# Optimization experiments

Measured on AMD Instinct MI355X. Metric: run time of the kernel, lower is better.

Reference implementation:

```python
import jax, jax.numpy as jnp
import numpy as np

ATT, WEMB, VIEW, ADIM, EMB = 312, 512, 16, 2048, 2048
B = 2048
IN = ATT + WEMB + VIEW * WEMB  # 9016; output_dim defaults to input_dim
EPS = 1e-8  # torch cosine_similarity eps


def setup_inputs() -> dict:
    key = jax.random.key(0)
    ks = jax.random.split(key, 8)
    s = 0.02
    return {
        "x": jax.random.normal(ks[0], (B, IN), dtype=jnp.float32),
        "Wq": s * jax.random.normal(ks[1], (WEMB, ADIM), dtype=jnp.float32),
        "bq": jnp.zeros((ADIM,), jnp.float32),
        "Wk": s * jax.random.normal(ks[2], (WEMB, ADIM), dtype=jnp.float32),
        "bk": jnp.zeros((ADIM,), jnp.float32),
        "Wv": s * jax.random.normal(ks[3], (WEMB, ADIM), dtype=jnp.float32),
        "bv": jnp.zeros((ADIM,), jnp.float32),
        "Wm": s * jax.random.normal(ks[4], (ATT + ADIM, EMB), dtype=jnp.float32),
        "bm": jnp.zeros((EMB,), jnp.float32),
        "Wd1": s * jax.random.normal(ks[5], (EMB, 4096), dtype=jnp.float32),
        "bd1": jnp.zeros((4096,), jnp.float32),
        "Wd2": s * jax.random.normal(ks[6], (4096, IN), dtype=jnp.float32),
        "bd2": jnp.zeros((IN,), jnp.float32),
    }


def reference(x, Wq, bq, Wk, bk, Wv, bv, Wm, bm, Wd1, bd1, Wd2, bd2):
    att_emb = x[:, :ATT]                                   # [B, 312]
    desc_emb = x[:, ATT:ATT + WEMB]                        # [B, 512]
    gpt_emb = x[:, ATT + WEMB:].reshape(x.shape[0], -1, WEMB)  # [B, V, 512]

    # q is the same projected desc for every view (expand before linear)
    q = desc_emb @ Wq + bq                                 # [B, A]
    k = jnp.einsum("bvw,wa->bva", gpt_emb, Wk) + bk        # [B, V, A]
    v = jnp.einsum("bvw,wa->bva", gpt_emb, Wv) + bv        # [B, V, A]

    # cosed score: cosine similarity * L2 distance
    dot = jnp.einsum("bva,ba->bv", k, q)                   # [B, V]
    qn = jnp.maximum(jnp.linalg.norm(q, axis=-1), EPS)     # [B]
    kn = jnp.maximum(jnp.linalg.norm(k, axis=-1), EPS)     # [B, V]
    cs = dot / (qn[:, None] * kn)
    ed = jnp.linalg.norm(q[:, None, :] - k, axis=-1)       # [B, V]
    attn = jax.nn.softmax(cs * ed, axis=-1)                # [B, V]

    # torch.matmul([B,V], [B,V,A]) -> [B,B,A]; .mean(dim=1) averages over the
    # attn-batch axis, i.e. fused[j] = mean_b(attn[b]) @ v[j]. Compute the
    # mathematically identical form without the BxBxA intermediate.
    attn_mean = attn.mean(axis=0)                          # [V]
    fused = jnp.einsum("v,bva->ba", attn_mean, v)          # [B, A]

    z = jax.nn.relu(jnp.concatenate([att_emb, fused], axis=1) @ Wm + bm)  # [B, EMB]
    h = jax.nn.relu(z @ Wd1 + bd1)                          # [B, 4096]
    return h @ Wd2 + bd2                                    # [B, IN]
```

## Files before the change

kernel.cpp:

```cpp
#include <hip/hip_runtime.h>


typedef __bf16 bf16x8 __attribute__((ext_vector_type(8)));
typedef float  f32x4  __attribute__((ext_vector_type(4)));
typedef unsigned short u16;

#define ATT   312
#define WEMB  512
#define VIEW  16
#define ADIM  2048
#define EMB   2048
#define BATCH 2048
#define INDIM 9016
#define KCAT  2360
#define KCATP 2432
#define NOUT  9016
#define NOUTP 9088

__device__ __forceinline__ u16 f2bf(float f) {
  unsigned u = __builtin_bit_cast(unsigned, f);
  u += 0x7FFFu + ((u >> 16) & 1u);
  return (u16)(u >> 16);
}

__device__ __forceinline__ void gl_lds16(const u16* g, u16* l) {
  __builtin_amdgcn_global_load_lds((const __attribute__((address_space(1))) void*)g,
                                   (__attribute__((address_space(3))) void*)l, 16, 0, 0);
}

__global__ void castx_k(const float* __restrict__ x, u16* __restrict__ cc,
                        u16* __restrict__ desc, u16* __restrict__ gpt) {
  const int b = blockIdx.x, t = threadIdx.x;
  const float4* row = (const float4*)(x + (size_t)b * INDIM);
  for (int c = t; c < INDIM / 4; c += 256) {
    float4 v = row[c];
    ushort4 o = make_ushort4(f2bf(v.x), f2bf(v.y), f2bf(v.z), f2bf(v.w));
    if (c < ATT / 4)                 *(ushort4*)&cc[(size_t)b * KCATP + c * 4] = o;
    else if (c < (ATT + WEMB) / 4)   *(ushort4*)&desc[(size_t)b * WEMB + (c - ATT / 4) * 4] = o;
    else                             *(ushort4*)&gpt[(size_t)b * (VIEW * WEMB) + (c - (ATT + WEMB) / 4) * 4] = o;
  }
}

__global__ void transcast_k(const float* __restrict__ src, u16* __restrict__ dst,
                            int K, int N, int Kp, int Np) {
  __shared__ float tile[64][65];
  const int k0 = blockIdx.y * 64, n0 = blockIdx.x * 64;
  const int t = threadIdx.x;
  const int tr = t >> 4, tc4 = (t & 15) * 4;
#pragma unroll
  for (int i = 0; i < 4; ++i) {
    const int k = k0 + tr + i * 16;
    float v0 = 0.f, v1 = 0.f, v2 = 0.f, v3 = 0.f;
    if (k < K) {
      const int n = n0 + tc4;
      const float* p = src + (size_t)k * N + n;
      if (n + 3 < N) { float4 v = *(const float4*)p; v0 = v.x; v1 = v.y; v2 = v.z; v3 = v.w; }
      else {
        if (n + 0 < N) v0 = p[0];
        if (n + 1 < N) v1 = p[1];
        if (n + 2 < N) v2 = p[2];
        if (n + 3 < N) v3 = p[3];
      }
    }
    tile[tr + i * 16][tc4 + 0] = v0;
    tile[tr + i * 16][tc4 + 1] = v1;
    tile[tr + i * 16][tc4 + 2] = v2;
    tile[tr + i * 16][tc4 + 3] = v3;
  }
  __syncthreads();
#pragma unroll
  for (int i = 0; i < 4; ++i) {
    const int rn = tr + i * 16;
    const int n = n0 + rn;
    const int kk = k0 + tc4;
    if (n < Np) {
      const bool nv = (n < N);
      ushort4 o = make_ushort4(f2bf(nv ? tile[tc4 + 0][rn] : 0.f),
                               f2bf(nv ? tile[tc4 + 1][rn] : 0.f),
                               f2bf(nv ? tile[tc4 + 2][rn] : 0.f),
                               f2bf(nv ? tile[tc4 + 3][rn] : 0.f));
      *(ushort4*)&dst[(size_t)n * Kp + kk] = o;
    }
  }
}

template <int MODE, bool RELU>
__global__ __launch_bounds__(256, 2)
void gemm_bt(const u16* __restrict__ A, const u16* __restrict__ BT,
             const float* __restrict__ bias, int K, int Nreal,
             float* __restrict__ dstF, u16* __restrict__ dstH, int ldc,
             const float* __restrict__ qbuf, float* __restrict__ dotb,
             float* __restrict__ kn2b, int mt, int nt, int fastm) {
  __shared__ alignas(16) u16 Ash[128 * 64];
  __shared__ alignas(16) u16 Bsh[128 * 64];
  const int nwg = mt * nt;
  const int xcd = blockIdx.x & 7, idx = blockIdx.x >> 3;
  const int qq = nwg >> 3, rr = nwg & 7;
  const int wg = (xcd < rr ? xcd * (qq + 1) : rr * (qq + 1) + (xcd - rr) * qq) + idx;
  int tm, tn;
  if (fastm) { tm = wg % mt; tn = wg / mt; } else { tn = wg % nt; tm = wg / nt; }

  const int tid = threadIdx.x;
  const int wave = tid >> 6, lane = tid & 63;
  const long m0 = (long)tm * 128;
  const long n0 = (long)tn * 128;
  const int wm = wave >> 1, wn = wave & 1;
  f32x4 acc[4][4] = {};

  const int srow = (wave << 5) + (lane >> 3);
  const int scol = (lane & 7) << 3;

  for (int k0 = 0; k0 < K; k0 += 64) {
    __syncthreads();
#pragma unroll
    for (int i = 0; i < 4; ++i) {
      const int r = srow + i * 8;
      gl_lds16(A + (m0 + r) * (long)K + k0 + scol, &Ash[r * 64 + scol]);
      gl_lds16(BT + (n0 + r) * (long)K + k0 + scol, &Bsh[r * 64 + scol]);
    }
    __syncthreads();
#pragma unroll
    for (int kb = 0; kb < 2; ++kb) {
      bf16x8 af[4], bfv[4];
#pragma unroll
      for (int f = 0; f < 4; ++f) {
        af[f]  = *(const bf16x8*)&Ash[(wm * 64 + f * 16 + (lane & 15)) * 64 + kb * 32 + (lane >> 4) * 8];
        bfv[f] = *(const bf16x8*)&Bsh[(wn * 64 + f * 16 + (lane & 15)) * 64 + kb * 32 + (lane >> 4) * 8];
      }
#pragma unroll
      for (int mf = 0; mf < 4; ++mf)
#pragma unroll
        for (int nf = 0; nf < 4; ++nf)
          acc[mf][nf] = __builtin_amdgcn_mfma_f32_16x16x32_bf16(af[mf], bfv[nf], acc[mf][nf], 0, 0, 0);
    }
  }

  const int lr = lane >> 4, lc = lane & 15;
  if (MODE == 2) {
#pragma unroll
    for (int mf = 0; mf < 4; ++mf) {
#pragma unroll
      for (int r = 0; r < 4; ++r) {
        const long grow = m0 + wm * 64 + mf * 16 + lr * 4 + r;
        const long b = grow >> 4;
        float ds = 0.f, ks = 0.f;
#pragma unroll
        for (int nf = 0; nf < 4; ++nf) {
          const long col = n0 + wn * 64 + nf * 16 + lc;
          float kv = acc[mf][nf][r] + bias[col];
          ds += kv * qbuf[b * ADIM + col];
          ks += kv * kv;
        }
#pragma unroll
        for (int m = 1; m < 16; m <<= 1) {
          ds += __shfl_xor(ds, m, 64);
          ks += __shfl_xor(ks, m, 64);
        }
        if (lc == 0) {
          atomicAdd(&dotb[grow], ds);
          atomicAdd(&kn2b[grow], ks);
        }
      }
    }
  } else {
#pragma unroll
    for (int mf = 0; mf < 4; ++mf) {
#pragma unroll
      for (int nf = 0; nf < 4; ++nf) {
        const long col = n0 + wn * 64 + nf * 16 + lc;
        if (col < Nreal) {
          const float bv_ = bias[col];
#pragma unroll
          for (int r = 0; r < 4; ++r) {
            const long row = m0 + wm * 64 + mf * 16 + lr * 4 + r;
            float v = acc[mf][nf][r] + bv_;
            if (RELU) v = fmaxf(v, 0.f);
            if (MODE == 0) dstF[row * (long)ldc + col] = v;
            else           dstH[row * (long)ldc + col] = f2bf(v);
          }
        }
      }
    }
  }
}

__global__ void qnorm_k(const float* __restrict__ q, float* __restrict__ qn2) {
  const int b = blockIdx.x, t = threadIdx.x;
  const float4* row = (const float4*)(q + (size_t)b * ADIM);
  float s = 0.f;
#pragma unroll
  for (int i = 0; i < 2; ++i) {
    float4 v = row[t + i * 256];
    s += v.x * v.x + v.y * v.y + v.z * v.z + v.w * v.w;
  }
#pragma unroll
  for (int m = 1; m < 64; m <<= 1) s += __shfl_xor(s, m, 64);
  __shared__ float wsum[4];
  if ((t & 63) == 0) wsum[t >> 6] = s;
  __syncthreads();
  if (t == 0) qn2[b] = wsum[0] + wsum[1] + wsum[2] + wsum[3];
}

__global__ void attn_k(const float* __restrict__ dotb, const float* __restrict__ kn2b,
                       const float* __restrict__ qn2, float* __restrict__ asum) {
  const int b = blockIdx.x * 256 + threadIdx.x;
  const int lane = threadIdx.x & 63;
  const float q2 = qn2[b];
  const float qn = fmaxf(sqrtf(q2), 1e-8f);
  float lg[VIEW];
  float mx = -1e30f;
#pragma unroll
  for (int v = 0; v < VIEW; ++v) {
    const float d = dotb[b * VIEW + v], k2 = kn2b[b * VIEW + v];
    const float kn = fmaxf(sqrtf(k2), 1e-8f);
    const float cs = d / (qn * kn);
    const float ed = sqrtf(fmaxf(q2 - 2.f * d + k2, 0.f));
    lg[v] = cs * ed;
    mx = fmaxf(mx, lg[v]);
  }
  float s = 0.f;
#pragma unroll
  for (int v = 0; v < VIEW; ++v) { lg[v] = expf(lg[v] - mx); s += lg[v]; }
  const float inv = 1.f / s;
#pragma unroll
  for (int v = 0; v < VIEW; ++v) {
    float a = lg[v] * inv;
#pragma unroll
    for (int m = 1; m < 64; m <<= 1) a += __shfl_xor(a, m, 64);
    if (lane == 0) atomicAdd(&asum[v], a);
  }
}

__global__ void gtilde_k(const float* __restrict__ x, const float* __restrict__ asum,
                         u16* __restrict__ g) {
  const int b = blockIdx.x, t = threadIdx.x;
  float am[VIEW];
#pragma unroll
  for (int v = 0; v < VIEW; ++v) am[v] = asum[v] * (1.f / (float)BATCH);
  const float* gx = x + (size_t)b * INDIM + (ATT + WEMB);
#pragma unroll
  for (int i = 0; i < 8; ++i) {
    const int w = i * 64 + t;
    float s = 0.f;
#pragma unroll
    for (int v = 0; v < VIEW; ++v) s += am[v] * gx[v * WEMB + w];
    g[(size_t)b * WEMB + w] = f2bf(s);
  }
}

extern "C" void kernel_launch(void* const* d_in, const int* in_sizes, int n_in,
                              void* d_out, int out_size, void* d_ws, size_t ws_size,
                              hipStream_t stream) {
  const float* x   = (const float*)d_in[0];
  const float* Wq  = (const float*)d_in[1];
  const float* bq  = (const float*)d_in[2];
  const float* Wk  = (const float*)d_in[3];
  const float* bk  = (const float*)d_in[4];
  const float* Wv  = (const float*)d_in[5];
  const float* bv  = (const float*)d_in[6];
  const float* Wm  = (const float*)d_in[7];
  const float* bm  = (const float*)d_in[8];
  const float* Wd1 = (const float*)d_in[9];
  const float* bd1 = (const float*)d_in[10];
  const float* Wd2 = (const float*)d_in[11];
  const float* bd2 = (const float*)d_in[12];
  float* out = (float*)d_out;

  char* ws = (char*)d_ws;
  size_t off = 0;
  auto alloc = [&](size_t bytes) -> void* {
    void* p = ws + off;
    off = (off + bytes + 255) & ~(size_t)255;
    return p;
  };
  u16* WqT  = (u16*)alloc((size_t)ADIM * WEMB * 2);
  u16* WkT  = (u16*)alloc((size_t)ADIM * WEMB * 2);
  u16* WvT  = (u16*)alloc((size_t)ADIM * WEMB * 2);
  u16* WmT  = (u16*)alloc((size_t)EMB * KCATP * 2);
  u16* Wd1T = (u16*)alloc((size_t)4096 * EMB * 2);
  u16* Wd2T = (u16*)alloc((size_t)NOUTP * 4096 * 2);
  u16* desc = (u16*)alloc((size_t)BATCH * WEMB * 2);
  u16* gpt  = (u16*)alloc((size_t)BATCH * VIEW * WEMB * 2);
  u16* cc   = (u16*)alloc((size_t)BATCH * KCATP * 2);
  float* q    = (float*)alloc((size_t)BATCH * ADIM * 4);
  float* qn2  = (float*)alloc((size_t)BATCH * 4);
  float* stats = (float*)alloc((size_t)(BATCH * VIEW * 2 + 64) * 4);
  float* dotb = stats;
  float* kn2b = stats + BATCH * VIEW;
  float* asum = stats + BATCH * VIEW * 2;
  u16* gt = (u16*)alloc((size_t)BATCH * WEMB * 2);
  u16* z  = (u16*)alloc((size_t)BATCH * EMB * 2);
  u16* h  = (u16*)alloc((size_t)BATCH * 4096 * 2);
  if (off > ws_size) return;

  hipMemsetAsync(stats, 0, (size_t)(BATCH * VIEW * 2 + 64) * 4, stream);
  hipMemsetAsync(cc, 0, (size_t)BATCH * KCATP * 2, stream);

  castx_k<<<BATCH, 256, 0, stream>>>(x, cc, desc, gpt);

  transcast_k<<<dim3(ADIM / 64, WEMB / 64), 256, 0, stream>>>(Wq, WqT, WEMB, ADIM, WEMB, ADIM);
  transcast_k<<<dim3(ADIM / 64, WEMB / 64), 256, 0, stream>>>(Wk, WkT, WEMB, ADIM, WEMB, ADIM);
  transcast_k<<<dim3(ADIM / 64, WEMB / 64), 256, 0, stream>>>(Wv, WvT, WEMB, ADIM, WEMB, ADIM);
  transcast_k<<<dim3(EMB / 64, KCATP / 64), 256, 0, stream>>>(Wm, WmT, KCAT, EMB, KCATP, EMB);
  transcast_k<<<dim3(4096 / 64, EMB / 64), 256, 0, stream>>>(Wd1, Wd1T, EMB, 4096, EMB, 4096);
  transcast_k<<<dim3(NOUTP / 64, 4096 / 64), 256, 0, stream>>>(Wd2, Wd2T, 4096, NOUT, 4096, NOUTP);

  gemm_bt<0, false><<<16 * 16, 256, 0, stream>>>(
      desc, WqT, bq, WEMB, ADIM, q, nullptr, ADIM, nullptr, nullptr, nullptr,
      BATCH / 128, ADIM / 128, 0);
  qnorm_k<<<BATCH, 256, 0, stream>>>(q, qn2);
  gemm_bt<2, false><<<256 * 16, 256, 0, stream>>>(
      gpt, WkT, bk, WEMB, ADIM, nullptr, nullptr, 0, q, dotb, kn2b,
      BATCH * VIEW / 128, ADIM / 128, 0);
  attn_k<<<BATCH / 256, 256, 0, stream>>>(dotb, kn2b, qn2, asum);
  gtilde_k<<<BATCH, 64, 0, stream>>>(x, asum, gt);
  gemm_bt<1, false><<<16 * 16, 256, 0, stream>>>(
      gt, WvT, bv, WEMB, ADIM, nullptr, cc + ATT, KCATP, nullptr, nullptr, nullptr,
      BATCH / 128, ADIM / 128, 0);
  gemm_bt<1, true><<<16 * 16, 256, 0, stream>>>(
      cc, WmT, bm, KCATP, EMB, nullptr, z, EMB, nullptr, nullptr, nullptr,
      BATCH / 128, EMB / 128, 0);
  gemm_bt<1, true><<<16 * 32, 256, 0, stream>>>(
      z, Wd1T, bd1, EMB, 4096, nullptr, h, 4096, nullptr, nullptr, nullptr,
      BATCH / 128, 4096 / 128, 1);
  gemm_bt<0, false><<<16 * 71, 256, 0, stream>>>(
      h, Wd2T, bd2, 4096, NOUT, out, nullptr, NOUT, nullptr, nullptr, nullptr,
      BATCH / 128, NOUTP / 128, 1);
}
```

Baseline: 713.2 us.

## Add 256x256 double-buffered 8-wave GEMM for large projections and decoder layers

Introduces a new 512-thread GEMM kernel with 256x256 tiles that double-buffers K slices in LDS. It uses swizzled LDS layout, interleaved global-to-LDS staging between MFMA quadrants with fine-grained waitcnt and barriers, and setprio around MFMA bursts. The kernel is used for the K-projection, Wd1 and Wd2 GEMMs, with the output padded to a multiple of 256. gtilde now reads the already-cast bf16 gpt buffer with vector loads instead of strided fp32 x. The large tiles use 128 KB of LDS and many accumulator registers, and the launch grids shrink (128 blocks for Wd1), which risks lower occupancy and tail imbalance.

```diff
diff --git a/kernel.cpp b/kernel.cpp
--- a/kernel.cpp
+++ b/kernel.cpp
@@ -15,7 +15,7 @@
 #define KCAT  2360
 #define KCATP 2432
 #define NOUT  9016
-#define NOUTP 9088
+#define NOUTP 9216
 
 __device__ __forceinline__ u16 f2bf(float f) {
   unsigned u = __builtin_bit_cast(unsigned, f);
@@ -84,15 +84,45 @@
   }
 }
 
+__device__ __forceinline__ void stage_half(const u16* __restrict__ src, int ld,
+                                           u16* dst, int wave, int lane) {
+#pragma unroll
+  for (int j = 0; j < 2; ++j) {
+    const int s = wave * 2 + j;
+    const int r = ((s >> 1) << 4) + (lane >> 2);
+    const int c = ((s & 1) << 5) +
+                  (((lane & 3) << 3) ^ (((lane >> 5) & 1) << 4));
+    gl_lds16(src + (long)r * ld + c, dst + s * 512 + (lane << 3));
+  }
+}
+
+#define BAR   __builtin_amdgcn_s_barrier()
+#define LGKM0 asm volatile("s_waitcnt lgkmcnt(0)" ::: "memory")
+#define VM6   asm volatile("s_waitcnt vmcnt(6)" ::: "memory")
+#define VM0   asm volatile("s_waitcnt vmcnt(0)" ::: "memory")
+
+#define RDA(bufo) do { _Pragma("unroll") for (int mf = 0; mf < 8; ++mf) \
+  _Pragma("unroll") for (int kk = 0; kk < 2; ++kk) \
+    a[mf][kk] = *(const bf16x8*)&lds[(bufo) + aoff0 + (mf * 2 + kk) * 512]; } while (0)
+#define RDB(bufo, nfa, nfb) do { _Pragma("unroll") for (int nf = (nfa); nf <= (nfb); ++nf) \
+  _Pragma("unroll") for (int kk = 0; kk < 2; ++kk) \
+    b[nf][kk] = *(const bf16x8*)&lds[(bufo) + boff0 + nf * 1024 + kk * 512]; } while (0)
+#define QUAD(qm, qn) do { __builtin_amdgcn_s_setprio(1); \
+  _Pragma("unroll") for (int m4 = 0; m4 < 4; ++m4) \
+  _Pragma("unroll") for (int n2 = 0; n2 < 2; ++n2) \
+  _Pragma("unroll") for (int kk = 0; kk < 2; ++kk) \
+    acc[(qm) * 4 + m4][(qn) * 2 + n2] = __builtin_amdgcn_mfma_f32_16x16x32_bf16( \
+        a[(qm) * 4 + m4][kk], b[(qn) * 2 + n2][kk], acc[(qm) * 4 + m4][(qn) * 2 + n2], 0, 0, 0); \
+  __builtin_amdgcn_s_setprio(0); } while (0)
+
 template <int MODE, bool RELU>
-__global__ __launch_bounds__(256, 2)
-void gemm_bt(const u16* __restrict__ A, const u16* __restrict__ BT,
+__global__ __launch_bounds__(512, 2)
+void gemm256(const u16* __restrict__ A, const u16* __restrict__ BT,
              const float* __restrict__ bias, int K, int Nreal,
              float* __restrict__ dstF, u16* __restrict__ dstH, int ldc,
              const float* __restrict__ qbuf, float* __restrict__ dotb,
              float* __restrict__ kn2b, int mt, int nt, int fastm) {
-  __shared__ alignas(16) u16 Ash[128 * 64];
-  __shared__ alignas(16) u16 Bsh[128 * 64];
+  __shared__ alignas(16) u16 lds[65536];
   const int nwg = mt * nt;
   const int xcd = blockIdx.x & 7, idx = blockIdx.x >> 3;
   const int qq = nwg >> 3, rr = nwg & 7;
@@ -102,53 +132,71 @@
 
   const int tid = threadIdx.x;
   const int wave = tid >> 6, lane = tid & 63;
-  const long m0 = (long)tm * 128;
-  const long n0 = (long)tn * 128;
-  const int wm = wave >> 1, wn = wave & 1;
-  f32x4 acc[4][4] = {};
-
-  const int srow = (wave << 5) + (lane >> 3);
-  const int scol = (lane & 7) << 3;
-
-  for (int k0 = 0; k0 < K; k0 += 64) {
-    __syncthreads();
-#pragma unroll
-    for (int i = 0; i < 4; ++i) {
-      const int r = srow + i * 8;
-      gl_lds16(A + (m0 + r) * (long)K + k0 + scol, &Ash[r * 64 + scol]);
-      gl_lds16(BT + (n0 + r) * (long)K + k0 + scol, &Bsh[r * 64 + scol]);
-    }
-    __syncthreads();
-#pragma unroll
-    for (int kb = 0; kb < 2; ++kb) {
-      bf16x8 af[4], bfv[4];
-#pragma unroll
-      for (int f = 0; f < 4; ++f) {
-        af[f]  = *(const bf16x8*)&Ash[(wm * 64 + f * 16 + (lane & 15)) * 64 + kb * 32 + (lane >> 4) * 8];
-        bfv[f] = *(const bf16x8*)&Bsh[(wn * 64 + f * 16 + (lane & 15)) * 64 + kb * 32 + (lane >> 4) * 8];
-      }
-#pragma unroll
-      for (int mf = 0; mf < 4; ++mf)
-#pragma unroll
-        for (int nf = 0; nf < 4; ++nf)
-          acc[mf][nf] = __builtin_amdgcn_mfma_f32_16x16x32_bf16(af[mf], bfv[nf], acc[mf][nf], 0, 0, 0);
-    }
+  const long m0 = (long)tm * 256, n0 = (long)tn * 256;
+  const int wm = wave >> 2, wn = wave & 3;
+  const u16* Ab = A + m0 * K;
+  const u16* Bb = BT + n0 * K;
+
+  f32x4 acc[8][4] = {};
+  bf16x8 a[8][2], b[4][2];
+  const int LP = (lane & 15) * 32 + ((((lane >> 4) << 3)) ^ (((lane >> 3) & 1) << 4));
+  const int aoff0 = wm * 8192 + LP;
+  const int boff0 = 16384 + (wn >> 1) * 8192 + (wn & 1) * 4096 + LP;
+  const int NT = K >> 6;
+
+  stage_half(Ab,               K, &lds[0],     wave, lane);
+  stage_half(Ab + 128 * K,     K, &lds[8192],  wave, lane);
+  stage_half(Bb,               K, &lds[16384], wave, lane);
+  stage_half(Bb + 128 * K,     K, &lds[24576], wave, lane);
+  stage_half(Ab + 64,          K, &lds[32768], wave, lane);
+  stage_half(Ab + 128 * K + 64, K, &lds[40960], wave, lane);
+  stage_half(Bb + 64,          K, &lds[49152], wave, lane);
+  VM6; BAR;
+
+  const int iters = NT >> 1;
+  for (int i = 0; i < iters; ++i) {
+    const int t0 = 2 * i;
+    const bool nl = (i < iters - 1);
+    RDA(0); RDB(0, 0, 1);
+    stage_half(Bb + 128 * K + (t0 + 1) * 64, K, &lds[57344], wave, lane);
+    BAR; LGKM0; QUAD(0, 0); BAR;
+    RDB(0, 2, 3);
+    if (nl) stage_half(Ab + (t0 + 2) * 64, K, &lds[0], wave, lane);
+    BAR; LGKM0; QUAD(1, 0); BAR;
+    if (nl) stage_half(Ab + 128 * K + (t0 + 2) * 64, K, &lds[8192], wave, lane);
+    BAR; QUAD(0, 1); BAR;
+    if (nl) stage_half(Bb + (t0 + 2) * 64, K, &lds[16384], wave, lane);
+    BAR; QUAD(1, 1);
+    if (nl) { VM6; } else { VM0; }
+    BAR;
+    RDA(32768); RDB(32768, 0, 1);
+    if (nl) stage_half(Bb + 128 * K + (t0 + 2) * 64, K, &lds[24576], wave, lane);
+    BAR; LGKM0; QUAD(0, 0); BAR;
+    RDB(32768, 2, 3);
+    if (nl) stage_half(Ab + (t0 + 3) * 64, K, &lds[32768], wave, lane);
+    BAR; LGKM0; QUAD(1, 0); BAR;
+    if (nl) stage_half(Ab + 128 * K + (t0 + 3) * 64, K, &lds[40960], wave, lane);
+    BAR; QUAD(0, 1); BAR;
+    if (nl) stage_half(Bb + (t0 + 3) * 64, K, &lds[49152], wave, lane);
+    BAR; QUAD(1, 1);
+    if (nl) VM6;
+    BAR;
   }
 
   const int lr = lane >> 4, lc = lane & 15;
   if (MODE == 2) {
 #pragma unroll
-    for (int mf = 0; mf < 4; ++mf) {
+    for (int mf = 0; mf < 8; ++mf) {
 #pragma unroll
       for (int r = 0; r < 4; ++r) {
-        const long grow = m0 + wm * 64 + mf * 16 + lr * 4 + r;
-        const long b = grow >> 4;
+        const long grow = m0 + wm * 128 + mf * 16 + lr * 4 + r;
+        const long bb = grow >> 4;
         float ds = 0.f, ks = 0.f;
 #pragma unroll
         for (int nf = 0; nf < 4; ++nf) {
           const long col = n0 + wn * 64 + nf * 16 + lc;
           float kv = acc[mf][nf][r] + bias[col];
-          ds += kv * qbuf[b * ADIM + col];
+          ds += kv * qbuf[bb * ADIM + col];
           ks += kv * kv;
         }
 #pragma unroll
@@ -164,7 +212,7 @@
     }
   } else {
 #pragma unroll
-    for (int mf = 0; mf < 4; ++mf) {
+    for (int mf = 0; mf < 8; ++mf) {
 #pragma unroll
       for (int nf = 0; nf < 4; ++nf) {
         const long col = n0 + wn * 64 + nf * 16 + lc;
@@ -172,12 +220,83 @@
           const float bv_ = bias[col];
 #pragma unroll
           for (int r = 0; r < 4; ++r) {
-            const long row = m0 + wm * 64 + mf * 16 + lr * 4 + r;
+            const long row = m0 + wm * 128 + mf * 16 + lr * 4 + r;
             float v = acc[mf][nf][r] + bv_;
             if (RELU) v = fmaxf(v, 0.f);
             if (MODE == 0) dstF[row * (long)ldc + col] = v;
             else           dstH[row * (long)ldc + col] = f2bf(v);
           }
+        }
+      }
+    }
+  }
+}
+
+template <int MODE, bool RELU>
+__global__ __launch_bounds__(256, 2)
+void gemm_bt(const u16* __restrict__ A, const u16* __restrict__ BT,
+             const float* __restrict__ bias, int K, int Nreal,
+             float* __restrict__ dstF, u16* __restrict__ dstH, int ldc,
+             int mt, int nt, int fastm) {
+  __shared__ alignas(16) u16 Ash[128 * 64];
+  __shared__ alignas(16) u16 Bsh[128 * 64];
+  const int nwg = mt * nt;
+  const int xcd = blockIdx.x & 7, idx = blockIdx.x >> 3;
+  const int qq = nwg >> 3, rr = nwg & 7;
+  const int wg = (xcd < rr ? xcd * (qq + 1) : rr * (qq + 1) + (xcd - rr) * qq) + idx;
+  int tm, tn;
+  if (fastm) { tm = wg % mt; tn = wg / mt; } else { tn = wg % nt; tm = wg / nt; }
+
+  const int tid = threadIdx.x;
+  const int wave = tid >> 6, lane = tid & 63;
+  const long m0 = (long)tm * 128;
+  const long n0 = (long)tn * 128;
+  const int wm = wave >> 1, wnn = wave & 1;
+  f32x4 acc[4][4] = {};
+
+  const int srow = (wave << 5) + (lane >> 3);
+  const int scol = (lane & 7) << 3;
+
+  for (int k0 = 0; k0 < K; k0 += 64) {
+    __syncthreads();
+#pragma unroll
+    for (int i = 0; i < 4; ++i) {
+      const int r = srow + i * 8;
+      gl_lds16(A + (m0 + r) * (long)K + k0 + scol, &Ash[r * 64 + scol]);
+      gl_lds16(BT + (n0 + r) * (long)K + k0 + scol, &Bsh[r * 64 + scol]);
+    }
+    __syncthreads();
+#pragma unroll
+    for (int kb = 0; kb < 2; ++kb) {
+      bf16x8 af[4], bfv[4];
+#pragma unroll
+      for (int f = 0; f < 4; ++f) {
+        af[f]  = *(const bf16x8*)&Ash[(wm * 64 + f * 16 + (lane & 15)) * 64 + kb * 32 + (lane >> 4) * 8];
+        bfv[f] = *(const bf16x8*)&Bsh[(wnn * 64 + f * 16 + (lane & 15)) * 64 + kb * 32 + (lane >> 4) * 8];
+      }
+#pragma unroll
+      for (int mf = 0; mf < 4; ++mf)
+#pragma unroll
+        for (int nf = 0; nf < 4; ++nf)
+          acc[mf][nf] = __builtin_amdgcn_mfma_f32_16x16x32_bf16(af[mf], bfv[nf], acc[mf][nf], 0, 0, 0);
+    }
+  }
+
+  const int lr = lane >> 4, lc = lane & 15;
+#pragma unroll
+  for (int mf = 0; mf < 4; ++mf) {
+#pragma unroll
+    for (int nf = 0; nf < 4; ++nf) {
+      const long col = n0 + wnn * 64 + nf * 16 + lc;
+      if (col < Nreal) {
+        const float bv_ = bias[col];
+#pragma unroll
+        for (int r = 0; r < 4; ++r) {
+          const long row = m0 + wm * 64 + mf * 16 + lr * 4 + r;
+          float v = acc[mf][nf][r] + bv_;
+          if (RELU) v = fmaxf(v, 0.f);
+          if (MODE == 0) dstF[row * (long)ldc + col] = v;
+          else           dstH[row * (long)ldc + col] = f2bf(v);
         }
       }
     }
@@ -224,28 +343,32 @@
   const float inv = 1.f / s;
 #pragma unroll
   for (int v = 0; v < VIEW; ++v) {
-    float a = lg[v] * inv;
-#pragma unroll
-    for (int m = 1; m < 64; m <<= 1) a += __shfl_xor(a, m, 64);
-    if (lane == 0) atomicAdd(&asum[v], a);
-  }
-}
-
-__global__ void gtilde_k(const float* __restrict__ x, const float* __restrict__ asum,
+    float aa = lg[v] * inv;
+#pragma unroll
+    for (int m = 1; m < 64; m <<= 1) aa += __shfl_xor(aa, m, 64);
+    if (lane == 0) atomicAdd(&asum[v], aa);
+  }
+}
+
+__global__ void gtilde_k(const u16* __restrict__ gpt, const float* __restrict__ asum,
                          u16* __restrict__ g) {
   const int b = blockIdx.x, t = threadIdx.x;
   float am[VIEW];
 #pragma unroll
   for (int v = 0; v < VIEW; ++v) am[v] = asum[v] * (1.f / (float)BATCH);
-  const float* gx = x + (size_t)b * INDIM + (ATT + WEMB);
-#pragma unroll
-  for (int i = 0; i < 8; ++i) {
-    const int w = i * 64 + t;
-    float s = 0.f;
-#pragma unroll
-    for (int v = 0; v < VIEW; ++v) s += am[v] * gx[v * WEMB + w];
-    g[(size_t)b * WEMB + w] = f2bf(s);
-  }
+  float s[8] = {};
+  const u16* gx = gpt + (size_t)b * (VIEW * WEMB) + t * 8;
+#pragma unroll
+  for (int v = 0; v < VIEW; ++v) {
+    bf16x8 gv = *(const bf16x8*)&gx[v * WEMB];
+#pragma unroll
+    for (int j = 0; j < 8; ++j) s[j] += am[v] * (float)gv[j];
+  }
+  ushort4 o0, o1;
+  o0 = make_ushort4(f2bf(s[0]), f2bf(s[1]), f2bf(s[2]), f2bf(s[3]));
+  o1 = make_ushort4(f2bf(s[4]), f2bf(s[5]), f2bf(s[6]), f2bf(s[7]));
+  *(ushort4*)&g[(size_t)b * WEMB + t * 8] = o0;
+  *(ushort4*)&g[(size_t)b * WEMB + t * 8 + 4] = o1;
 }
 
 extern "C" void kernel_launch(void* const* d_in, const int* in_sizes, int n_in,
@@ -306,24 +429,21 @@
   transcast_k<<<dim3(NOUTP / 64, 4096 / 64), 256, 0, stream>>>(Wd2, Wd2T, 4096, NOUT, 4096, NOUTP);
 
   gemm_bt<0, false><<<16 * 16, 256, 0, stream>>>(
-      desc, WqT, bq, WEMB, ADIM, q, nullptr, ADIM, nullptr, nullptr, nullptr,
-      BATCH / 128, ADIM / 128, 0);
+      desc, WqT, bq, WEMB, ADIM, q, nullptr, ADIM, BATCH / 128, ADIM / 128, 0);
   qnorm_k<<<BATCH, 256, 0, stream>>>(q, qn2);
-  gemm_bt<2, false><<<256 * 16, 256, 0, stream>>>(
+  gemm256<2, false><<<128 * 8, 512, 0, stream>>>(
       gpt, WkT, bk, WEMB, ADIM, nullptr, nullptr, 0, q, dotb, kn2b,
-      BATCH * VIEW / 128, ADIM / 128, 0);
+      BATCH * VIEW / 256, ADIM / 256, 0);
   attn_k<<<BATCH / 256, 256, 0, stream>>>(dotb, kn2b, qn2, asum);
-  gtilde_k<<<BATCH, 64, 0, stream>>>(x, asum, gt);
+  gtilde_k<<<BATCH, 64, 0, stream>>>(gpt, asum, gt);
   gemm_bt<1, false><<<16 * 16, 256, 0, stream>>>(
-      gt, WvT, bv, WEMB, ADIM, nullptr, cc + ATT, KCATP, nullptr, nullptr, nullptr,
-      BATCH / 128, ADIM / 128, 0);
+      gt, WvT, bv, WEMB, ADIM, nullptr, cc + ATT, KCATP, BATCH / 128, ADIM / 128, 0);
   gemm_bt<1, true><<<16 * 16, 256, 0, stream>>>(
-      cc, WmT, bm, KCATP, EMB, nullptr, z, EMB, nullptr, nullptr, nullptr,
-      BATCH / 128, EMB / 128, 0);
-  gemm_bt<1, true><<<16 * 32, 256, 0, stream>>>(
+      cc, WmT, bm, KCATP, EMB, nullptr, z, EMB, BATCH / 128, EMB / 128, 0);
+  gemm256<1, true><<<8 * 16, 512, 0, stream>>>(
       z, Wd1T, bd1, EMB, 4096, nullptr, h, 4096, nullptr, nullptr, nullptr,
-      BATCH / 128, 4096 / 128, 1);
-  gemm_bt<0, false><<<16 * 71, 256, 0, stream>>>(
+      BATCH / 256, 4096 / 256, 0);
+  gemm256<0, false><<<8 * 36, 512, 0, stream>>>(
       h, Wd2T, bd2, 4096, NOUT, out, nullptr, NOUT, nullptr, nullptr, nullptr,
-      BATCH / 128, NOUTP / 128, 1);
-}
+      BATCH / 256, NOUTP / 256, 1);
+}
```

Result: no change. 700.3 us (-1.8%).
